# Optimization experiments

Measured on AMD Instinct MI355X. Metric: run time of the kernel, lower is better.

## Reference

```python
import jax, jax.numpy as jnp
import numpy as np

# Irreps: in/out = 48x0e + 16x1o (dim 96), sh = 1x0e + 1x1o (dim 4)
N, E = 4096, 32768
NS, NV, NEF = 48, 16, 128
# FullyConnectedTensorProduct paths: (0e,0e->0e) 48*48, (1o,1o->0e) 16*48,
# (0e,1o->1o) 48*16, (1o,0e->1o) 16*16  => weight_numel = 4096
W_SS, W_VS, W_SV, W_VV = NS * NS, NV * NS, NS * NV, NV * NV
WNUM = W_SS + W_VS + W_SV + W_VV
EPS = 1e-5
INV_SQRT3 = 1.0 / np.sqrt(3.0)
ALPHA = 1.0 / np.sqrt(64.0)  # path norm: fan_in = 48*1 + 16*1 = 64 per output irrep


def setup_inputs() -> dict:
    key = jax.random.key(0)
    ks = jax.random.split(key, 10)
    node_attr = jax.random.normal(ks[0], (N, NS + 3 * NV), dtype=jnp.float32)
    edge_index = jax.random.randint(ks[1], (2, E), 0, N, dtype=jnp.int64)
    edge_attr = jax.random.normal(ks[2], (E, NEF), dtype=jnp.float32)
    edge_sh = jax.random.normal(ks[3], (E, 4), dtype=jnp.float32)
    fc_w1 = jax.random.normal(ks[4], (NEF, NEF), dtype=jnp.float32) / np.sqrt(NEF)
    fc_b1 = jnp.zeros((NEF,), dtype=jnp.float32)
    fc_w2 = jax.random.normal(ks[5], (NEF, WNUM), dtype=jnp.float32) / np.sqrt(NEF)
    fc_b2 = jnp.zeros((WNUM,), dtype=jnp.float32)
    bn_weight = jnp.ones((NS + NV,), dtype=jnp.float32)
    bn_bias = jnp.zeros((NS,), dtype=jnp.float32)
    return {"node_attr": node_attr, "edge_index": edge_index, "edge_attr": edge_attr,
            "edge_sh": edge_sh, "fc_w1": fc_w1, "fc_b1": fc_b1, "fc_w2": fc_w2,
            "fc_b2": fc_b2, "bn_weight": bn_weight, "bn_bias": bn_bias}


def _dlrelu(x):
    # DoubleleakyRelu: identity for |x|<=10, slope 0.01 outside
    return jnp.where(jnp.abs(x) <= 10.0, x, 0.01 * x)


def _forward(node_attr, edge_attr, edge_sh, fc_w1, fc_b1, fc_w2, fc_b2,
             bn_weight, bn_bias, src, dst):
    # edge MLP -> per-edge TP weights (dropout=0 -> identity)
    h = jax.nn.relu(edge_attr @ fc_w1 + fc_b1)
    w = _dlrelu(h @ fc_w2 + fc_b2)  # [E, 4096]
    w_ss = w[:, :W_SS].reshape(E, NS, NS)
    w_vs = w[:, W_SS:W_SS + W_VS].reshape(E, NV, NS)
    w_sv = w[:, W_SS + W_VS:W_SS + W_VS + W_SV].reshape(E, NS, NV)
    w_vv = w[:, W_SS + W_VS + W_SV:].reshape(E, NV, NV)

    # gather source node features; split into scalar / vector irreps
    x = node_attr[src]                     # [E, 96]
    xs = x[:, :NS]                         # [E, 48]
    xv = x[:, NS:].reshape(E, NV, 3)       # [E, 16, 3]
    ss = edge_sh[:, 0]                     # [E]
    sv = edge_sh[:, 1:4]                   # [E, 3]

    # CG tensor product (l<=1), per-path weights
    dot = jnp.einsum('eim,em->ei', xv, sv) * INV_SQRT3          # 1o x 1o -> 0e
    out_s = ALPHA * (jnp.einsum('ei,eik->ek', xs * ss[:, None], w_ss)
                     + jnp.einsum('ei,eik->ek', dot, w_vs))      # [E, 48]
    out_v = ALPHA * (jnp.einsum('ei,eik,em->ekm', xs, w_sv, sv)  # 0e x 1o -> 1o
                     + jnp.einsum('eim,eik->ekm', xv, w_vv) * ss[:, None, None])  # [E,16,3]

    msg = jnp.concatenate([out_s, out_v.reshape(E, 3 * NV)], axis=-1)  # [E, 96]
    out = jax.ops.segment_sum(msg, dst, num_segments=N)                # scatter sum
    out = out + node_attr                                              # residual (same dim)

    # e3nn-style BatchNorm (training mode, component normalization)
    s = out[:, :NS]
    v = out[:, NS:].reshape(N, NV, 3)
    s_c = s - jnp.mean(s, axis=0)
    s_norm = jnp.mean(s_c * s_c, axis=0)                    # [48]
    s_out = s_c * ((s_norm + EPS) ** -0.5 * bn_weight[:NS]) + bn_bias
    v_norm = jnp.mean(v * v, axis=(0, 2))                   # [16]
    v_out = v * ((v_norm + EPS) ** -0.5 * bn_weight[NS:])[None, :, None]
    return jnp.concatenate([s_out, v_out.reshape(N, 3 * NV)], axis=-1)


def reference(node_attr, edge_index, edge_attr, edge_sh, fc_w1, fc_b1, fc_w2,
              fc_b2, bn_weight, bn_bias):
    src, dst = edge_index[0], edge_index[1]
    return _forward(node_attr, edge_attr, edge_sh, fc_w1, fc_b1, fc_w2, fc_b2,
                    bn_weight, bn_bias, src, dst)
```

## Files before the change

### kernel.cpp

```cpp
#include <hip/hip_runtime.h>
#include <hip/hip_bf16.h>

#define NNODES 4096
#define NEDGES 32768
#define CH 96
#define EPS 1e-5f
#define INV_SQRT3 0.57735026918962576f
#define ALPHA 0.125f

#define EB 32
#define NBLK (NEDGES / EB)

#define OFF_MSG 0
#define OFF_ST  393216
#define OFF_WSB 393344
#define WSB_W2_U16 (OFF_WSB * 2)
#define WSB_W1_U16 (WSB_W2_U16 + 524288)
#define WS_BYTES1 (393330 * 4)
#define WS_BYTES2 (393344 * 4 + 524288 * 2 + 16384 * 2)

typedef __attribute__((ext_vector_type(8))) short short8;
typedef __attribute__((ext_vector_type(4))) float floatx4;

__device__ __forceinline__ unsigned short f2bf(float f) {
  union { float f; unsigned int u; } v; v.f = f;
  return (unsigned short)((v.u + 0x7FFFu + ((v.u >> 16) & 1u)) >> 16);
}
__device__ __forceinline__ float bf2f(unsigned short u) {
  union { unsigned int i; float f; } v; v.i = ((unsigned int)u) << 16; return v.f;
}
__device__ __forceinline__ float fin(float x) {
  return (x == x && fabsf(x) < 1e30f) ? x : 0.f;
}
__device__ __forceinline__ float dlrelu(float g) {
  return (fabsf(g) <= 10.f) ? g : 0.01f * g;
}

__global__ __launch_bounds__(256) void k0_prep(const float* w1, const float* w2,
                                               float* ws, int ok1, int ok2) {
  __shared__ float tile[128 * 16];
  const int t = threadIdx.x;
  const int b = blockIdx.x;
  unsigned short* wsu = (unsigned short*)ws;

  if (ok1) {
    for (int i = b * 256 + t; i < 393330; i += 256 * 256) ws[i] = 0.f;
  }
  if (ok2) {
    {
      const int T = b;
#pragma unroll
      for (int p = 0; p < 8; p++) {
        int k = p * 16 + (t >> 4), col = t & 15;
        tile[k * 16 + col] = w2[(size_t)k * 4096 + T * 16 + col];
      }
      __syncthreads();
      int s = t >> 6, lane = t & 63, q = (lane >> 4), cl = lane & 15;
      unsigned int r[4];
#pragma unroll
      for (int jj = 0; jj < 4; jj++) {
        int k0 = s * 32 + q * 8 + 2 * jj;
        unsigned int lo = f2bf(tile[k0 * 16 + cl]);
        unsigned int hi = f2bf(tile[(k0 + 1) * 16 + cl]);
        r[jj] = lo | (hi << 16);
      }
      *(uint4*)(wsu + WSB_W2_U16 + ((size_t)(T * 4 + s) * 64 + lane) * 8) =
          make_uint4(r[0], r[1], r[2], r[3]);
    }
    if (b < 8) {
      __syncthreads();
      const int T = b;
#pragma unroll
      for (int p = 0; p < 8; p++) {
        int k = p * 16 + (t >> 4), col = t & 15;
        tile[k * 16 + col] = w1[(size_t)k * 128 + T * 16 + col];
      }
      __syncthreads();
      int s = t >> 6, lane = t & 63, q = (lane >> 4), cl = lane & 15;
      unsigned int r[4];
#pragma unroll
      for (int jj = 0; jj < 4; jj++) {
        int k0 = s * 32 + q * 8 + 2 * jj;
        unsigned int lo = f2bf(tile[k0 * 16 + cl]);
        unsigned int hi = f2bf(tile[(k0 + 1) * 16 + cl]);
        r[jj] = lo | (hi << 16);
      }
      *(uint4*)(wsu + WSB_W1_U16 + ((size_t)(T * 4 + s) * 64 + lane) * 8) =
          make_uint4(r[0], r[1], r[2], r[3]);
    }
  }
}

__global__ __launch_bounds__(256, 4) void k1_fused(const int* eidx, const float* na,
                                                   const float* ea, const float* esh,
                                                   const float* b1g, const float* b2g,
                                                   float* ws, int ok2) {
  if (!ok2) return;
  __shared__ __align__(16) unsigned short a_lds[EB * 161];
  __shared__ __align__(16) char ovl[8704];
  __shared__ float ss_lds[EB];
  __shared__ float sv_lds[EB][3];
  __shared__ int dst_lds[EB];
  __shared__ int src_lds[EB];
  unsigned short* hscr = (unsigned short*)ovl;
  float* tmp_l = (float*)ovl;
  float* vv_l  = (float*)(ovl + 2176);

  const int tid = threadIdx.x;
  const int lane = tid & 63;
  const int q = lane >> 4;
  const int cl = lane & 15;
  const int wv = tid >> 6;
  const int e0 = blockIdx.x * EB;
  unsigned short* wsu = (unsigned short*)ws;
  float* msg = ws;

  if (tid < EB) {
    int o = 0;
    for (int i = 1; i < 256; i += 2) o |= eidx[i];
    const int is64 = (o == 0);
    int e = e0 + tid;
    int s = is64 ? eidx[2 * e] : eidx[e];
    int d = is64 ? eidx[2 * (NEDGES + e)] : eidx[NEDGES + e];
    src_lds[tid] = s & (NNODES - 1);
    dst_lds[tid] = d & (NNODES - 1);
    float4 sh = *(const float4*)(esh + (size_t)e * 4);
    ss_lds[tid] = sh.x;
    sv_lds[tid][0] = sh.y; sv_lds[tid][1] = sh.z; sv_lds[tid][2] = sh.w;
  }
  __syncthreads();

  for (int idx = tid; idx < EB * 160; idx += 256) {
    int e = idx / 160, i = idx - e * 160;
    const float* x = na + (size_t)src_lds[e] * CH;
    float v;
    if (i < 48) v = x[i] * ss_lds[e];
    else if (i < 64) {
      int ii = i - 48;
      v = (x[48 + 3 * ii] * sv_lds[e][0] + x[49 + 3 * ii] * sv_lds[e][1] +
           x[50 + 3 * ii] * sv_lds[e][2]) * INV_SQRT3;
    } else if (i < 112) v = x[i - 64];
    else v = x[48 + (i - 112)];
    a_lds[e * 161 + i] = f2bf(v);
  }

  {
    short8 a1[2][4];
#pragma unroll
    for (int mt = 0; mt < 2; mt++)
#pragma unroll
      for (int ks = 0; ks < 4; ks++) {
        const float* src = ea + (size_t)(e0 + mt * 16 + cl) * 128 + ks * 32 + q * 8;
        float4 v0 = *(const float4*)src;
        float4 v1 = *(const float4*)(src + 4);
        union { short8 s; unsigned int u[4]; } pk;
        pk.u[0] = f2bf(v0.x) | ((unsigned)f2bf(v0.y) << 16);
        pk.u[1] = f2bf(v0.z) | ((unsigned)f2bf(v0.w) << 16);
        pk.u[2] = f2bf(v1.x) | ((unsigned)f2bf(v1.y) << 16);
        pk.u[3] = f2bf(v1.z) | ((unsigned)f2bf(v1.w) << 16);
        a1[mt][ks] = pk.s;
      }
    const short8* w1f = (const short8*)(wsu + WSB_W1_U16);
#pragma unroll
    for (int t = 0; t < 2; t++) {
      int nt = wv * 2 + t;
      int hcol = nt * 16 + cl;
      float hb = b1g[hcol];
      floatx4 c0 = (floatx4)(hb), c1 = (floatx4)(hb);
#pragma unroll
      for (int ks = 0; ks < 4; ks++) {
        short8 bf = w1f[(nt * 4 + ks) * 64 + lane];
        c0 = __builtin_amdgcn_mfma_f32_16x16x32_bf16(a1[0][ks], bf, c0, 0, 0, 0);
        c1 = __builtin_amdgcn_mfma_f32_16x16x32_bf16(a1[1][ks], bf, c1, 0, 0, 0);
      }
#pragma unroll
      for (int r = 0; r < 4; r++) {
        hscr[(q * 4 + r) * 136 + hcol] = f2bf(fmaxf(c0[r], 0.f));
        hscr[(16 + q * 4 + r) * 136 + hcol] = f2bf(fmaxf(c1[r], 0.f));
      }
    }
  }
  __syncthreads();

  short8 areg[2][4];
#pragma unroll
  for (int mt = 0; mt < 2; mt++)
#pragma unroll
    for (int ks = 0; ks < 4; ks++)
      areg[mt][ks] = *(const short8*)&hscr[(mt * 16 + cl) * 136 + ks * 32 + q * 8];
  __syncthreads();

  const short8* w2f = (const short8*)(wsu + WSB_W2_U16);

#define LOADB(dst, bdst, uu) { const short8* _p = w2f + (size_t)((uu)&255) * 256 + lane; \
    dst[0] = _p[0]; dst[1] = _p[64]; dst[2] = _p[128]; dst[3] = _p[192]; \
    bdst = b2g[((uu)&255) * 16 + cl]; }

#define MFMA8(bb, bsc, c0, c1) \
    floatx4 c0 = (floatx4)(bsc), c1 = (floatx4)(bsc); \
    _Pragma("unroll") \
    for (int ks = 0; ks < 4; ks++) { \
      c0 = __builtin_amdgcn_mfma_f32_16x16x32_bf16(areg[0][ks], bb[ks], c0, 0, 0, 0); \
      c1 = __builtin_amdgcn_mfma_f32_16x16x32_bf16(areg[1][ks], bb[ks], c1, 0, 0, 0); }

  if (wv < 3) {
    const int ng = (wv == 2) ? 22 : 21;
    const int base_ai = wv * 21;
    const int u0 = base_ai * 3;
    float accS[3][2][4];
#pragma unroll
    for (int c = 0; c < 3; c++)
#pragma unroll
      for (int mt = 0; mt < 2; mt++)
#pragma unroll
        for (int r = 0; r < 4; r++) accS[c][mt][r] = 0.f;

    short8 b0[4], b1[4], b2[4];
    float bb0, bb1, bb2;
    LOADB(b0, bb0, u0); LOADB(b1, bb1, u0 + 1);
    for (int g = 0; g < ng; g++) {
      const int ai = base_ai + g;
      const int u = u0 + 3 * g;
      float av[2][4];
#pragma unroll
      for (int mt = 0; mt < 2; mt++)
#pragma unroll
        for (int r = 0; r < 4; r++)
          av[mt][r] = bf2f(a_lds[(mt * 16 + q * 4 + r) * 161 + ai]);

#define COMP_SS(bb, bsc, cidx) { \
      MFMA8(bb, bsc, c0, c1); \
      _Pragma("unroll") \
      for (int r = 0; r < 4; r++) { \
        accS[cidx][0][r] += av[0][r] * dlrelu(c0[r]); \
        accS[cidx][1][r] += av[1][r] * dlrelu(c1[r]); } }

      LOADB(b2, bb2, u + 2); COMP_SS(b0, bb0, 0);
      LOADB(b0, bb0, u + 3); COMP_SS(b1, bb1, 1);
      LOADB(b1, bb1, u + 4); COMP_SS(b2, bb2, 2);
    }
#pragma unroll
    for (int mt = 0; mt < 2; mt++)
#pragma unroll
      for (int r = 0; r < 4; r++) {
        int e = mt * 16 + q * 4 + r;
        float* mrow = msg + (size_t)dst_lds[e] * CH;
#pragma unroll
        for (int c = 0; c < 3; c++)
          atomicAdd(mrow + c * 16 + cl, ALPHA * accS[c][mt][r]);
      }
  } else {
    float accT[2][4], accV[2][4][3];
#pragma unroll
    for (int mt = 0; mt < 2; mt++)
#pragma unroll
      for (int r = 0; r < 4; r++) {
        accT[mt][r] = 0.f;
        accV[mt][r][0] = 0.f; accV[mt][r][1] = 0.f; accV[mt][r][2] = 0.f;
      }
    short8 b0[4], b1[4];
    float bb0, bb1;

#define COMP_SV(bb, bsc, uu) { \
    const int ai = (uu) - 128; \
    MFMA8(bb, bsc, c0, c1); \
    _Pragma("unroll") \
    for (int r = 0; r < 4; r++) { \
      accT[0][r] += bf2f(a_lds[(q * 4 + r) * 161 + ai]) * dlrelu(c0[r]); \
      accT[1][r] += bf2f(a_lds[(16 + q * 4 + r) * 161 + ai]) * dlrelu(c1[r]); } }

#define COMP_VV(bb, bsc, uu) { \
    const int ab = 3 * (uu) - 608; \
    MFMA8(bb, bsc, c0, c1); \
    _Pragma("unroll") \
    for (int r = 0; r < 4; r++) { \
      float w0 = dlrelu(c0[r]), w1v = dlrelu(c1[r]); \
      int ba0 = (q * 4 + r) * 161 + ab, ba1 = (16 + q * 4 + r) * 161 + ab; \
      accV[0][r][0] += bf2f(a_lds[ba0 + 0]) * w0; \
      accV[0][r][1] += bf2f(a_lds[ba0 + 1]) * w0; \
      accV[0][r][2] += bf2f(a_lds[ba0 + 2]) * w0; \
      accV[1][r][0] += bf2f(a_lds[ba1 + 0]) * w1v; \
      accV[1][r][1] += bf2f(a_lds[ba1 + 1]) * w1v; \
      accV[1][r][2] += bf2f(a_lds[ba1 + 2]) * w1v; } }

    LOADB(b0, bb0, 192);
    for (int i = 0; i < 48; i += 2) {
      const int u = 192 + i;
      LOADB(b1, bb1, u + 1); COMP_SV(b0, bb0, u);
      LOADB(b0, bb0, u + 2); COMP_SV(b1, bb1, u + 1);
    }
    for (int i = 0; i < 16; i += 2) {
      const int u = 240 + i;
      LOADB(b1, bb1, u + 1); COMP_VV(b0, bb0, u);
      LOADB(b0, bb0, u + 2); COMP_VV(b1, bb1, u + 1);
    }
#pragma unroll
    for (int mt = 0; mt < 2; mt++)
#pragma unroll
      for (int r = 0; r < 4; r++) {
        int e = mt * 16 + q * 4 + r;
        tmp_l[e * 17 + cl] = accT[mt][r];
#pragma unroll
        for (int m = 0; m < 3; m++)
          vv_l[e * 49 + 3 * cl + m] = accV[mt][r][m];
      }
  }
  __syncthreads();

  for (int idx = tid; idx < EB * 48; idx += 256) {
    int e = idx / 48, t2 = idx - e * 48;
    int k = t2 / 3, m = t2 - k * 3;
    float val = ALPHA * (tmp_l[e * 17 + k] * sv_lds[e][m] +
                         ss_lds[e] * vv_l[e * 49 + 3 * k + m]);
    atomicAdd(msg + (size_t)dst_lds[e] * CH + 48 + t2, val);
  }
}

__global__ __launch_bounds__(256) void k23_fused(const float* na, const float* bnw,
                                                 const float* bnb, float* ws,
                                                 float* out, int ok1) {
  __shared__ float part[112];
  __shared__ float mean_s[48], scale_s[48], bias_s[48], scale_v[16];
  float* msg = ws + OFF_MSG;
  float* st = ws + OFF_ST;
  const int tid = threadIdx.x;
  const int stride = gridDim.x * 256;

  if (ok1) {
    for (int i = tid; i < 112; i += 256) part[i] = 0.f;
    __syncthreads();
    for (int idx = blockIdx.x * 256 + tid; idx < NNODES * CH; idx += stride) {
      int c = idx % CH;
      float t = msg[idx] + na[idx];
      if (c < 48) { atomicAdd(&part[c], t); atomicAdd(&part[48 + c], t * t); }
      else { int k = (c - 48) / 3; atomicAdd(&part[96 + k], t * t); }
    }
    __syncthreads();
    for (int i = tid; i < 112; i += 256) atomicAdd(&st[i], part[i]);
    __syncthreads();
    if (tid == 0) {
      __threadfence();
      int* ctr = (int*)(st + 112);
      atomicAdd(ctr, 1);
      while (__hip_atomic_load(ctr, __ATOMIC_ACQUIRE, __HIP_MEMORY_SCOPE_AGENT) <
             (int)gridDim.x) {}
    }
    __syncthreads();
  }

  if (tid < 48) {
    float s1 = ok1 ? fin(__hip_atomic_load(&st[tid], __ATOMIC_RELAXED,
                                           __HIP_MEMORY_SCOPE_AGENT)) : 0.f;
    float s2 = ok1 ? fin(__hip_atomic_load(&st[48 + tid], __ATOMIC_RELAXED,
                                           __HIP_MEMORY_SCOPE_AGENT)) : 0.f;
    float m = s1 * (1.f / NNODES);
    float var = fmaxf(s2 * (1.f / NNODES) - m * m, 0.f);
    mean_s[tid] = m;
    scale_s[tid] = rsqrtf(var + EPS) * bnw[tid];
    bias_s[tid] = bnb[tid];
  } else if (tid < 64) {
    int k = tid - 48;
    float s2 = ok1 ? fin(__hip_atomic_load(&st[96 + k], __ATOMIC_RELAXED,
                                           __HIP_MEMORY_SCOPE_AGENT)) : 0.f;
    scale_v[k] = rsqrtf(fmaxf(s2 * (1.f / (3.f * NNODES)), 0.f) + EPS) * bnw[48 + k];
  }
  __syncthreads();
  for (int idx = blockIdx.x * 256 + tid; idx < NNODES * CH; idx += stride) {
    int c = idx % CH;
    float t = (ok1 ? msg[idx] : 0.f) + na[idx];
    float o;
    if (c < 48) o = (t - mean_s[c]) * scale_s[c] + bias_s[c];
    else { int k = (c - 48) / 3; o = t * scale_v[k]; }
    out[idx] = fin(o);
  }
}

extern "C" void kernel_launch(void* const* d_in, const int* in_sizes, int n_in,
                              void* d_out, int out_size, void* d_ws, size_t ws_size,
                              hipStream_t stream) {
  const float* na  = (const float*)d_in[0];
  const int* eidx  = (const int*)d_in[1];
  const float* ea  = (const float*)d_in[2];
  const float* esh = (const float*)d_in[3];
  const float* w1  = (const float*)d_in[4];
  const float* b1  = (const float*)d_in[5];
  const float* w2  = (const float*)d_in[6];
  const float* b2  = (const float*)d_in[7];
  const float* bnw = (const float*)d_in[8];
  const float* bnb = (const float*)d_in[9];
  float* out = (float*)d_out;
  float* ws = (float*)d_ws;
  const int ok1 = (ws_size >= (size_t)WS_BYTES1) ? 1 : 0;
  const int ok2 = (ws_size >= (size_t)WS_BYTES2) ? 1 : 0;

  hipLaunchKernelGGL(k0_prep,   dim3(256), dim3(256), 0, stream, w1, w2, ws, ok1, ok2);
  hipLaunchKernelGGL(k1_fused,  dim3(NBLK), dim3(256), 0, stream,
                     eidx, na, ea, esh, b1, b2, ws, ok2);
  hipLaunchKernelGGL(k23_fused, dim3(512), dim3(256), 0, stream,
                     na, bnw, bnb, ws, out, ok1);
}
```

Before: 211.0 us.

## Split each edge block's weight columns across two workgroups and split BN kernel

Doubles the edge-kernel grid so each 32-edge tile is handled by two workgroups: one computes part of the scalar-scalar paths, the other the remaining scalar paths plus the vector paths, with four waves sharing the work and partial sums combined through LDS atomics. This rebalances the previously idle fourth wave and adds occupancy, at the cost of recomputing the edge MLP hidden layer twice per tile. The fused stats/normalize kernel with its spin-wait grid barrier is replaced by two separate launches, which trades the barrier for an extra kernel launch.

New measurement: 225.7 us. 1.07x slower.

```diff
diff --git a/kernel.cpp b/kernel.cpp
--- a/kernel.cpp
+++ b/kernel.cpp
@@ -9,14 +9,14 @@
 #define ALPHA 0.125f
 
 #define EB 32
-#define NBLK (NEDGES / EB)
+#define NEBLK (NEDGES / EB)
 
 #define OFF_MSG 0
 #define OFF_ST  393216
 #define OFF_WSB 393344
 #define WSB_W2_U16 (OFF_WSB * 2)
 #define WSB_W1_U16 (WSB_W2_U16 + 524288)
-#define WS_BYTES1 (393330 * 4)
+#define WS_BYTES1 (393328 * 4)
 #define WS_BYTES2 (393344 * 4 + 524288 * 2 + 16384 * 2)
 
 typedef __attribute__((ext_vector_type(8))) short short8;
@@ -44,7 +44,7 @@
   unsigned short* wsu = (unsigned short*)ws;
 
   if (ok1) {
-    for (int i = b * 256 + t; i < 393330; i += 256 * 256) ws[i] = 0.f;
+    for (int i = b * 256 + t; i < 393328; i += 256 * 256) ws[i] = 0.f;
   }
   if (ok2) {
     {
@@ -111,7 +111,8 @@
   const int q = lane >> 4;
   const int cl = lane & 15;
   const int wv = tid >> 6;
-  const int e0 = blockIdx.x * EB;
+  const int h = blockIdx.x & 1;
+  const int e0 = (blockIdx.x >> 1) * EB;
   unsigned short* wsu = (unsigned short*)ws;
   float* msg = ws;
 
@@ -130,18 +131,33 @@
   }
   __syncthreads();
 
-  for (int idx = tid; idx < EB * 160; idx += 256) {
-    int e = idx / 160, i = idx - e * 160;
-    const float* x = na + (size_t)src_lds[e] * CH;
-    float v;
-    if (i < 48) v = x[i] * ss_lds[e];
-    else if (i < 64) {
-      int ii = i - 48;
-      v = (x[48 + 3 * ii] * sv_lds[e][0] + x[49 + 3 * ii] * sv_lds[e][1] +
-           x[50 + 3 * ii] * sv_lds[e][2]) * INV_SQRT3;
-    } else if (i < 112) v = x[i - 64];
-    else v = x[48 + (i - 112)];
-    a_lds[e * 161 + i] = f2bf(v);
+  if (h == 0) {
+    for (int idx = tid; idx < EB * 64; idx += 256) {
+      int e = idx >> 6, i = idx & 63;
+      const float* x = na + (size_t)src_lds[e] * CH;
+      float v;
+      if (i < 48) v = x[i] * ss_lds[e];
+      else {
+        int ii = i - 48;
+        v = (x[48 + 3 * ii] * sv_lds[e][0] + x[49 + 3 * ii] * sv_lds[e][1] +
+             x[50 + 3 * ii] * sv_lds[e][2]) * INV_SQRT3;
+      }
+      a_lds[e * 161 + i] = f2bf(v);
+    }
+  } else {
+    for (int idx = tid; idx < EB * 128; idx += 256) {
+      int e = idx >> 7, i = 32 + (idx & 127);
+      const float* x = na + (size_t)src_lds[e] * CH;
+      float v;
+      if (i < 48) v = x[i] * ss_lds[e];
+      else if (i < 64) {
+        int ii = i - 48;
+        v = (x[48 + 3 * ii] * sv_lds[e][0] + x[49 + 3 * ii] * sv_lds[e][1] +
+             x[50 + 3 * ii] * sv_lds[e][2]) * INV_SQRT3;
+      } else if (i < 112) v = x[i - 64];
+      else v = x[48 + (i - 112)];
+      a_lds[e * 161 + i] = f2bf(v);
+    }
   }
 
   {
@@ -190,6 +206,11 @@
       areg[mt][ks] = *(const short8*)&hscr[(mt * 16 + cl) * 136 + ks * 32 + q * 8];
   __syncthreads();
 
+  if (h == 1) {
+    for (int idx = tid; idx < EB * 17; idx += 256) tmp_l[idx] = 0.f;
+  }
+  __syncthreads();
+
   const short8* w2f = (const short8*)(wsu + WSB_W2_U16);
 
 #define LOADB(dst, bdst, uu) { const short8* _p = w2f + (size_t)((uu)&255) * 256 + lane; \
@@ -203,9 +224,11 @@
       c0 = __builtin_amdgcn_mfma_f32_16x16x32_bf16(areg[0][ks], bb[ks], c0, 0, 0, 0); \
       c1 = __builtin_amdgcn_mfma_f32_16x16x32_bf16(areg[1][ks], bb[ks], c1, 0, 0, 0); }
 
-  if (wv < 3) {
-    const int ng = (wv == 2) ? 22 : 21;
-    const int base_ai = wv * 21;
+  const int is_ss = (h == 0) || (wv < 2);
+  if (is_ss) {
+    const int base_ai = (h == 0) ? ((wv < 2) ? wv * 11 : 22 + (wv - 2) * 10)
+                                 : 42 + wv * 11;
+    const int ng = (h == 0 && wv >= 2) ? 10 : 11;
     const int u0 = base_ai * 3;
     float accS[3][2][4];
 #pragma unroll
@@ -283,76 +306,81 @@
       accV[1][r][1] += bf2f(a_lds[ba1 + 1]) * w1v; \
       accV[1][r][2] += bf2f(a_lds[ba1 + 2]) * w1v; } }
 
-    LOADB(b0, bb0, 192);
-    for (int i = 0; i < 48; i += 2) {
-      const int u = 192 + i;
-      LOADB(b1, bb1, u + 1); COMP_SV(b0, bb0, u);
-      LOADB(b0, bb0, u + 2); COMP_SV(b1, bb1, u + 1);
-    }
-    for (int i = 0; i < 16; i += 2) {
-      const int u = 240 + i;
-      LOADB(b1, bb1, u + 1); COMP_VV(b0, bb0, u);
-      LOADB(b0, bb0, u + 2); COMP_VV(b1, bb1, u + 1);
+    if (wv == 2) {
+      LOADB(b0, bb0, 192);
+      for (int i = 0; i < 36; i += 2) {
+        const int u = 192 + i;
+        LOADB(b1, bb1, u + 1); COMP_SV(b0, bb0, u);
+        LOADB(b0, bb0, u + 2); COMP_SV(b1, bb1, u + 1);
+      }
+    } else {
+      LOADB(b0, bb0, 228);
+      for (int i = 0; i < 12; i += 2) {
+        const int u = 228 + i;
+        LOADB(b1, bb1, u + 1); COMP_SV(b0, bb0, u);
+        LOADB(b0, bb0, u + 2); COMP_SV(b1, bb1, u + 1);
+      }
+      for (int i = 0; i < 16; i += 2) {
+        const int u = 240 + i;
+        LOADB(b1, bb1, u + 1); COMP_VV(b0, bb0, u);
+        LOADB(b0, bb0, u + 2); COMP_VV(b1, bb1, u + 1);
+      }
     }
 #pragma unroll
     for (int mt = 0; mt < 2; mt++)
 #pragma unroll
       for (int r = 0; r < 4; r++) {
         int e = mt * 16 + q * 4 + r;
-        tmp_l[e * 17 + cl] = accT[mt][r];
-#pragma unroll
-        for (int m = 0; m < 3; m++)
-          vv_l[e * 49 + 3 * cl + m] = accV[mt][r][m];
-      }
-  }
-  __syncthreads();
-
-  for (int idx = tid; idx < EB * 48; idx += 256) {
-    int e = idx / 48, t2 = idx - e * 48;
-    int k = t2 / 3, m = t2 - k * 3;
-    float val = ALPHA * (tmp_l[e * 17 + k] * sv_lds[e][m] +
-                         ss_lds[e] * vv_l[e * 49 + 3 * k + m]);
-    atomicAdd(msg + (size_t)dst_lds[e] * CH + 48 + t2, val);
-  }
-}
-
-__global__ __launch_bounds__(256) void k23_fused(const float* na, const float* bnw,
-                                                 const float* bnb, float* ws,
-                                                 float* out, int ok1) {
+        atomicAdd(&tmp_l[e * 17 + cl], accT[mt][r]);
+        if (wv == 3) {
+#pragma unroll
+          for (int m = 0; m < 3; m++)
+            vv_l[e * 49 + 3 * cl + m] = accV[mt][r][m];
+        }
+      }
+  }
+  __syncthreads();
+
+  if (h == 1) {
+    for (int idx = tid; idx < EB * 48; idx += 256) {
+      int e = idx / 48, t2 = idx - e * 48;
+      int k = t2 / 3, m = t2 - k * 3;
+      float val = ALPHA * (tmp_l[e * 17 + k] * sv_lds[e][m] +
+                           ss_lds[e] * vv_l[e * 49 + 3 * k + m]);
+      atomicAdd(msg + (size_t)dst_lds[e] * CH + 48 + t2, val);
+    }
+  }
+}
+
+__global__ __launch_bounds__(256) void k2_stats(const float* na, float* ws, int ok1) {
   __shared__ float part[112];
-  __shared__ float mean_s[48], scale_s[48], bias_s[48], scale_v[16];
-  float* msg = ws + OFF_MSG;
+  const float* msg = ws + OFF_MSG;
   float* st = ws + OFF_ST;
-  const int tid = threadIdx.x;
-  const int stride = gridDim.x * 256;
-
+  for (int i = threadIdx.x; i < 112; i += 256) part[i] = 0.f;
+  __syncthreads();
   if (ok1) {
-    for (int i = tid; i < 112; i += 256) part[i] = 0.f;
-    __syncthreads();
-    for (int idx = blockIdx.x * 256 + tid; idx < NNODES * CH; idx += stride) {
+    int stride = gridDim.x * 256;
+    for (int idx = blockIdx.x * 256 + threadIdx.x; idx < NNODES * CH; idx += stride) {
       int c = idx % CH;
       float t = msg[idx] + na[idx];
       if (c < 48) { atomicAdd(&part[c], t); atomicAdd(&part[48 + c], t * t); }
       else { int k = (c - 48) / 3; atomicAdd(&part[96 + k], t * t); }
     }
     __syncthreads();
-    for (int i = tid; i < 112; i += 256) atomicAdd(&st[i], part[i]);
-    __syncthreads();
-    if (tid == 0) {
-      __threadfence();
-      int* ctr = (int*)(st + 112);
-      atomicAdd(ctr, 1);
-      while (__hip_atomic_load(ctr, __ATOMIC_ACQUIRE, __HIP_MEMORY_SCOPE_AGENT) <
-             (int)gridDim.x) {}
-    }
-    __syncthreads();
-  }
-
+    for (int i = threadIdx.x; i < 112; i += 256) atomicAdd(&st[i], part[i]);
+  }
+}
+
+__global__ __launch_bounds__(256) void k3_final(const float* na, const float* bnw,
+                                                const float* bnb, const float* ws,
+                                                float* out, int ok1) {
+  __shared__ float mean_s[48], scale_s[48], bias_s[48], scale_v[16];
+  const float* msg = ws + OFF_MSG;
+  const float* st = ws + OFF_ST;
+  const int tid = threadIdx.x;
   if (tid < 48) {
-    float s1 = ok1 ? fin(__hip_atomic_load(&st[tid], __ATOMIC_RELAXED,
-                                           __HIP_MEMORY_SCOPE_AGENT)) : 0.f;
-    float s2 = ok1 ? fin(__hip_atomic_load(&st[48 + tid], __ATOMIC_RELAXED,
-                                           __HIP_MEMORY_SCOPE_AGENT)) : 0.f;
+    float s1 = ok1 ? fin(st[tid]) : 0.f;
+    float s2 = ok1 ? fin(st[48 + tid]) : 0.f;
     float m = s1 * (1.f / NNODES);
     float var = fmaxf(s2 * (1.f / NNODES) - m * m, 0.f);
     mean_s[tid] = m;
@@ -360,11 +388,11 @@
     bias_s[tid] = bnb[tid];
   } else if (tid < 64) {
     int k = tid - 48;
-    float s2 = ok1 ? fin(__hip_atomic_load(&st[96 + k], __ATOMIC_RELAXED,
-                                           __HIP_MEMORY_SCOPE_AGENT)) : 0.f;
+    float s2 = ok1 ? fin(st[96 + k]) : 0.f;
     scale_v[k] = rsqrtf(fmaxf(s2 * (1.f / (3.f * NNODES)), 0.f) + EPS) * bnw[48 + k];
   }
   __syncthreads();
+  int stride = gridDim.x * 256;
   for (int idx = blockIdx.x * 256 + tid; idx < NNODES * CH; idx += stride) {
     int c = idx % CH;
     float t = (ok1 ? msg[idx] : 0.f) + na[idx];
@@ -393,9 +421,9 @@
   const int ok1 = (ws_size >= (size_t)WS_BYTES1) ? 1 : 0;
   const int ok2 = (ws_size >= (size_t)WS_BYTES2) ? 1 : 0;
 
-  hipLaunchKernelGGL(k0_prep,   dim3(256), dim3(256), 0, stream, w1, w2, ws, ok1, ok2);
-  hipLaunchKernelGGL(k1_fused,  dim3(NBLK), dim3(256), 0, stream,
+  hipLaunchKernelGGL(k0_prep,  dim3(256), dim3(256), 0, stream, w1, w2, ws, ok1, ok2);
+  hipLaunchKernelGGL(k1_fused, dim3(NEBLK * 2), dim3(256), 0, stream,
                      eidx, na, ea, esh, b1, b2, ws, ok2);
-  hipLaunchKernelGGL(k23_fused, dim3(512), dim3(256), 0, stream,
-                     na, bnw, bnb, ws, out, ok1);
-}
+  hipLaunchKernelGGL(k2_stats, dim3(512), dim3(256), 0, stream, na, ws, ok1);
+  hipLaunchKernelGGL(k3_final, dim3(512), dim3(256), 0, stream, na, bnw, bnb, ws, out, ok1);
+}
```

## Transpose gathered edge features to fp32 LDS and split stats/finalize kernels

Applied to the files above, without the earlier changes.

The gathered per-edge activation matrix now sits in LDS as fp32, transposed to feature-major with a padded stride. The scalar, SV and VV paths read four edges at once with float4 loads instead of many scalar bf16 loads and conversions, and the scalar path prefetches the next column. The fused stats/normalize kernel, which relied on a spin-wait grid barrier, is split into two kernel launches, so the barrier counter is gone. This uses more LDS per block and adds one launch, which may affect occupancy of the main kernel.

New measurement: 255.1 us. +20.9%, slower.

```diff
diff --git a/kernel.cpp b/kernel.cpp
--- a/kernel.cpp
+++ b/kernel.cpp
@@ -16,7 +16,7 @@
 #define OFF_WSB 393344
 #define WSB_W2_U16 (OFF_WSB * 2)
 #define WSB_W1_U16 (WSB_W2_U16 + 524288)
-#define WS_BYTES1 (393330 * 4)
+#define WS_BYTES1 (393328 * 4)
 #define WS_BYTES2 (393344 * 4 + 524288 * 2 + 16384 * 2)
 
 typedef __attribute__((ext_vector_type(8))) short short8;
@@ -25,9 +25,6 @@
 __device__ __forceinline__ unsigned short f2bf(float f) {
   union { float f; unsigned int u; } v; v.f = f;
   return (unsigned short)((v.u + 0x7FFFu + ((v.u >> 16) & 1u)) >> 16);
-}
-__device__ __forceinline__ float bf2f(unsigned short u) {
-  union { unsigned int i; float f; } v; v.i = ((unsigned int)u) << 16; return v.f;
 }
 __device__ __forceinline__ float fin(float x) {
   return (x == x && fabsf(x) < 1e30f) ? x : 0.f;
@@ -44,7 +41,7 @@
   unsigned short* wsu = (unsigned short*)ws;
 
   if (ok1) {
-    for (int i = b * 256 + t; i < 393330; i += 256 * 256) ws[i] = 0.f;
+    for (int i = b * 256 + t; i < 393328; i += 256 * 256) ws[i] = 0.f;
   }
   if (ok2) {
     {
@@ -96,7 +93,7 @@
                                                    const float* b1g, const float* b2g,
                                                    float* ws, int ok2) {
   if (!ok2) return;
-  __shared__ __align__(16) unsigned short a_lds[EB * 161];
+  __shared__ __align__(16) float a_ldsT[160 * 36];
   __shared__ __align__(16) char ovl[8704];
   __shared__ float ss_lds[EB];
   __shared__ float sv_lds[EB][3];
@@ -130,8 +127,8 @@
   }
   __syncthreads();
 
-  for (int idx = tid; idx < EB * 160; idx += 256) {
-    int e = idx / 160, i = idx - e * 160;
+  for (int idx = tid; idx < 160 * EB; idx += 256) {
+    int i = idx >> 5, e = idx & 31;
     const float* x = na + (size_t)src_lds[e] * CH;
     float v;
     if (i < 48) v = x[i] * ss_lds[e];
@@ -141,7 +138,7 @@
            x[50 + 3 * ii] * sv_lds[e][2]) * INV_SQRT3;
     } else if (i < 112) v = x[i - 64];
     else v = x[48 + (i - 112)];
-    a_lds[e * 161 + i] = f2bf(v);
+    a_ldsT[i * 36 + e] = v;
   }
 
   {
@@ -218,26 +215,25 @@
     short8 b0[4], b1[4], b2[4];
     float bb0, bb1, bb2;
     LOADB(b0, bb0, u0); LOADB(b1, bb1, u0 + 1);
+    float4 av0 = *(const float4*)&a_ldsT[base_ai * 36 + q * 4];
+    float4 av1 = *(const float4*)&a_ldsT[base_ai * 36 + 16 + q * 4];
     for (int g = 0; g < ng; g++) {
-      const int ai = base_ai + g;
       const int u = u0 + 3 * g;
-      float av[2][4];
-#pragma unroll
-      for (int mt = 0; mt < 2; mt++)
-#pragma unroll
-        for (int r = 0; r < 4; r++)
-          av[mt][r] = bf2f(a_lds[(mt * 16 + q * 4 + r) * 161 + ai]);
+      const int ain = base_ai + ((g + 1 < ng) ? g + 1 : g);
+      float4 nav0 = *(const float4*)&a_ldsT[ain * 36 + q * 4];
+      float4 nav1 = *(const float4*)&a_ldsT[ain * 36 + 16 + q * 4];
 
 #define COMP_SS(bb, bsc, cidx) { \
       MFMA8(bb, bsc, c0, c1); \
       _Pragma("unroll") \
       for (int r = 0; r < 4; r++) { \
-        accS[cidx][0][r] += av[0][r] * dlrelu(c0[r]); \
-        accS[cidx][1][r] += av[1][r] * dlrelu(c1[r]); } }
+        accS[cidx][0][r] += av0[r] * dlrelu(c0[r]); \
+        accS[cidx][1][r] += av1[r] * dlrelu(c1[r]); } }
 
       LOADB(b2, bb2, u + 2); COMP_SS(b0, bb0, 0);
       LOADB(b0, bb0, u + 3); COMP_SS(b1, bb1, 1);
       LOADB(b1, bb1, u + 4); COMP_SS(b2, bb2, 2);
+      av0 = nav0; av1 = nav1;
     }
 #pragma unroll
     for (int mt = 0; mt < 2; mt++)
@@ -263,25 +259,25 @@
 
 #define COMP_SV(bb, bsc, uu) { \
     const int ai = (uu) - 128; \
+    float4 sv0 = *(const float4*)&a_ldsT[ai * 36 + q * 4]; \
+    float4 sv1 = *(const float4*)&a_ldsT[ai * 36 + 16 + q * 4]; \
     MFMA8(bb, bsc, c0, c1); \
     _Pragma("unroll") \
     for (int r = 0; r < 4; r++) { \
-      accT[0][r] += bf2f(a_lds[(q * 4 + r) * 161 + ai]) * dlrelu(c0[r]); \
-      accT[1][r] += bf2f(a_lds[(16 + q * 4 + r) * 161 + ai]) * dlrelu(c1[r]); } }
+      accT[0][r] += sv0[r] * dlrelu(c0[r]); \
+      accT[1][r] += sv1[r] * dlrelu(c1[r]); } }
 
 #define COMP_VV(bb, bsc, uu) { \
     const int ab = 3 * (uu) - 608; \
     MFMA8(bb, bsc, c0, c1); \
     _Pragma("unroll") \
-    for (int r = 0; r < 4; r++) { \
-      float w0 = dlrelu(c0[r]), w1v = dlrelu(c1[r]); \
-      int ba0 = (q * 4 + r) * 161 + ab, ba1 = (16 + q * 4 + r) * 161 + ab; \
-      accV[0][r][0] += bf2f(a_lds[ba0 + 0]) * w0; \
-      accV[0][r][1] += bf2f(a_lds[ba0 + 1]) * w0; \
-      accV[0][r][2] += bf2f(a_lds[ba0 + 2]) * w0; \
-      accV[1][r][0] += bf2f(a_lds[ba1 + 0]) * w1v; \
-      accV[1][r][1] += bf2f(a_lds[ba1 + 1]) * w1v; \
-      accV[1][r][2] += bf2f(a_lds[ba1 + 2]) * w1v; } }
+    for (int m = 0; m < 3; m++) { \
+      float4 vv0 = *(const float4*)&a_ldsT[(ab + m) * 36 + q * 4]; \
+      float4 vv1 = *(const float4*)&a_ldsT[(ab + m) * 36 + 16 + q * 4]; \
+      _Pragma("unroll") \
+      for (int r = 0; r < 4; r++) { \
+        accV[0][r][m] += vv0[r] * dlrelu(c0[r]); \
+        accV[1][r][m] += vv1[r] * dlrelu(c1[r]); } } }
 
     LOADB(b0, bb0, 192);
     for (int i = 0; i < 48; i += 2) {
@@ -316,43 +312,35 @@
   }
 }
 
-__global__ __launch_bounds__(256) void k23_fused(const float* na, const float* bnw,
-                                                 const float* bnb, float* ws,
-                                                 float* out, int ok1) {
+__global__ __launch_bounds__(256) void k2_stats(const float* na, float* ws, int ok1) {
   __shared__ float part[112];
-  __shared__ float mean_s[48], scale_s[48], bias_s[48], scale_v[16];
-  float* msg = ws + OFF_MSG;
+  const float* msg = ws + OFF_MSG;
   float* st = ws + OFF_ST;
-  const int tid = threadIdx.x;
-  const int stride = gridDim.x * 256;
-
+  for (int i = threadIdx.x; i < 112; i += 256) part[i] = 0.f;
+  __syncthreads();
   if (ok1) {
-    for (int i = tid; i < 112; i += 256) part[i] = 0.f;
-    __syncthreads();
-    for (int idx = blockIdx.x * 256 + tid; idx < NNODES * CH; idx += stride) {
+    int stride = gridDim.x * 256;
+    for (int idx = blockIdx.x * 256 + threadIdx.x; idx < NNODES * CH; idx += stride) {
       int c = idx % CH;
       float t = msg[idx] + na[idx];
       if (c < 48) { atomicAdd(&part[c], t); atomicAdd(&part[48 + c], t * t); }
       else { int k = (c - 48) / 3; atomicAdd(&part[96 + k], t * t); }
     }
     __syncthreads();
-    for (int i = tid; i < 112; i += 256) atomicAdd(&st[i], part[i]);
-    __syncthreads();
-    if (tid == 0) {
-      __threadfence();
-      int* ctr = (int*)(st + 112);
-      atomicAdd(ctr, 1);
-      while (__hip_atomic_load(ctr, __ATOMIC_ACQUIRE, __HIP_MEMORY_SCOPE_AGENT) <
-             (int)gridDim.x) {}
-    }
-    __syncthreads();
-  }
-
+    for (int i = threadIdx.x; i < 112; i += 256) atomicAdd(&st[i], part[i]);
+  }
+}
+
+__global__ __launch_bounds__(256) void k3_final(const float* na, const float* bnw,
+                                                const float* bnb, const float* ws,
+                                                float* out, int ok1) {
+  __shared__ float mean_s[48], scale_s[48], bias_s[48], scale_v[16];
+  const float* msg = ws + OFF_MSG;
+  const float* st = ws + OFF_ST;
+  const int tid = threadIdx.x;
   if (tid < 48) {
-    float s1 = ok1 ? fin(__hip_atomic_load(&st[tid], __ATOMIC_RELAXED,
-                                           __HIP_MEMORY_SCOPE_AGENT)) : 0.f;
-    float s2 = ok1 ? fin(__hip_atomic_load(&st[48 + tid], __ATOMIC_RELAXED,
-                                           __HIP_MEMORY_SCOPE_AGENT)) : 0.f;
+    float s1 = ok1 ? fin(st[tid]) : 0.f;
+    float s2 = ok1 ? fin(st[48 + tid]) : 0.f;
     float m = s1 * (1.f / NNODES);
     float var = fmaxf(s2 * (1.f / NNODES) - m * m, 0.f);
     mean_s[tid] = m;
@@ -360,11 +348,11 @@
     bias_s[tid] = bnb[tid];
   } else if (tid < 64) {
     int k = tid - 48;
-    float s2 = ok1 ? fin(__hip_atomic_load(&st[96 + k], __ATOMIC_RELAXED,
-                                           __HIP_MEMORY_SCOPE_AGENT)) : 0.f;
+    float s2 = ok1 ? fin(st[96 + k]) : 0.f;
     scale_v[k] = rsqrtf(fmaxf(s2 * (1.f / (3.f * NNODES)), 0.f) + EPS) * bnw[48 + k];
   }
   __syncthreads();
+  int stride = gridDim.x * 256;
   for (int idx = blockIdx.x * 256 + tid; idx < NNODES * CH; idx += stride) {
     int c = idx % CH;
     float t = (ok1 ? msg[idx] : 0.f) + na[idx];
@@ -393,9 +381,9 @@
   const int ok1 = (ws_size >= (size_t)WS_BYTES1) ? 1 : 0;
   const int ok2 = (ws_size >= (size_t)WS_BYTES2) ? 1 : 0;
 
-  hipLaunchKernelGGL(k0_prep,   dim3(256), dim3(256), 0, stream, w1, w2, ws, ok1, ok2);
-  hipLaunchKernelGGL(k1_fused,  dim3(NBLK), dim3(256), 0, stream,
+  hipLaunchKernelGGL(k0_prep,  dim3(256), dim3(256), 0, stream, w1, w2, ws, ok1, ok2);
+  hipLaunchKernelGGL(k1_fused, dim3(NBLK), dim3(256), 0, stream,
                      eidx, na, ea, esh, b1, b2, ws, ok2);
-  hipLaunchKernelGGL(k23_fused, dim3(512), dim3(256), 0, stream,
-                     na, bnw, bnb, ws, out, ok1);
-}
+  hipLaunchKernelGGL(k2_stats, dim3(512), dim3(256), 0, stream, na, ws, ok1);
+  hipLaunchKernelGGL(k3_final, dim3(512), dim3(256), 0, stream, na, bnw, bnb, ws, out, ok1);
+}
```
